# Performance work log

Hardware: AMD Instinct MI355X
Metric: run time of the kernel (lower is better)

## Reference

```python
import jax, jax.numpy as jnp
import numpy as np

N = 50000
E = 800000
C_IN, C_HID, C_OUT = 512, 128, 2
HEADS2 = 3
NEG_SLOPE = 0.2


def gat_conv(x, src, dst, W, att_src, att_dst, bias, heads, ch, concat):
    """PyG GATConv (eval mode) on pre-augmented (self-loop included) edge lists.
    x: [N, F_in], W: [F_in, heads*ch], att_*: [heads, ch], bias: [heads*ch] or [ch].
    """
    n = x.shape[0]
    h = (x @ W).reshape(n, heads, ch)                 # [N, H, C]
    a_src = (h * att_src).sum(-1)                     # [N, H]
    a_dst = (h * att_dst).sum(-1)                     # [N, H]
    e = jax.nn.leaky_relu(a_src[src] + a_dst[dst], NEG_SLOPE)  # [E', H]
    # segment softmax over edges sharing a destination node
    m = jax.ops.segment_max(e, dst, num_segments=n)
    m = jnp.where(jnp.isfinite(m), m, 0.0)
    ex = jnp.exp(e - m[dst])
    denom = jax.ops.segment_sum(ex, dst, num_segments=n)
    alpha = ex / (denom[dst] + 1e-16)                 # [E', H]
    out = jax.ops.segment_sum(h[src] * alpha[:, :, None], dst, num_segments=n)  # [N, H, C]
    out = out.reshape(n, heads * ch) if concat else out.mean(axis=1)
    return out + bias


def setup_inputs() -> dict:
    key = jax.random.key(0)
    ks = jax.random.split(key, 12)
    x = jax.random.normal(ks[0], (N, C_IN), dtype=jnp.float32)
    edge_index = jax.random.randint(ks[1], (2, E), 0, N, dtype=jnp.int64)
    s1 = 1.0 / np.sqrt(C_IN)
    s2 = 1.0 / np.sqrt(C_HID)
    return {
        "x": x,
        "edge_index": edge_index,
        "W1": jax.random.normal(ks[2], (C_IN, C_HID), dtype=jnp.float32) * s1,
        "att_src1": jax.random.normal(ks[3], (1, C_HID), dtype=jnp.float32) * s2,
        "att_dst1": jax.random.normal(ks[4], (1, C_HID), dtype=jnp.float32) * s2,
        "bias1": jnp.zeros((C_HID,), dtype=jnp.float32),
        "W2": jax.random.normal(ks[5], (C_HID, HEADS2 * C_OUT), dtype=jnp.float32) * s2,
        "att_src2": jax.random.normal(ks[6], (HEADS2, C_OUT), dtype=jnp.float32) * 0.5,
        "att_dst2": jax.random.normal(ks[7], (HEADS2, C_OUT), dtype=jnp.float32) * 0.5,
        "bias2": jnp.zeros((C_OUT,), dtype=jnp.float32),
    }


def reference(x, edge_index, W1, att_src1, att_dst1, bias1, W2, att_src2, att_dst2, bias2):
    n = x.shape[0]
    loop = jnp.arange(n, dtype=edge_index.dtype)
    src = jnp.concatenate([edge_index[0], loop])      # PyG add_self_loops=True
    dst = jnp.concatenate([edge_index[1], loop])
    h = gat_conv(x, src, dst, W1, att_src1, att_dst1, bias1, 1, C_HID, True)
    h = jax.nn.relu(h)                                # Dropout is identity in eval
    out = gat_conv(h, src, dst, W2, att_src2, att_dst2, bias2, HEADS2, C_OUT, False)
    return out
```

## Files before the change

### kernel.cpp

```cpp
#include <hip/hip_runtime.h>

#define N_NODES 50000
#define N_EDGES 800000
#define E_TOT   850000
#define C_IN    512
#define C_HID   128
#define NEG     0.2f

typedef _Float16 f16x8 __attribute__((ext_vector_type(8)));
typedef __attribute__((ext_vector_type(4))) float f32x4;

__device__ __forceinline__ float leaky(float x) { return x > 0.f ? x : NEG * x; }

union U32H2 { unsigned u; _Float16 h[2]; float f; };
union BFrag { uint4 u; f16x8 h; };

__device__ __forceinline__ unsigned short f2h(float f) {
  U32H2 c; c.h[0] = (_Float16)f; return (unsigned short)(c.u & 0xffff);
}

__device__ __forceinline__ unsigned pk2h(float a, float b) {
  union { __fp16 v __attribute__((ext_vector_type(2))); unsigned u; } c;
  c.v = __builtin_amdgcn_cvt_pkrtz(a, b);
  return c.u;
}

__global__ __launch_bounds__(256) void setup_kernel(
    const float* __restrict__ W1, const float* __restrict__ as1,
    const float* __restrict__ ad1, const int* __restrict__ ei,
    unsigned short* __restrict__ Wswz, float* __restrict__ v1s, float* __restrict__ v1d,
    int* __restrict__ deg, int* __restrict__ rnk) {
  const int b = blockIdx.x;
  if (b < 32) {
    int t = b * 256 + threadIdx.x;
    int c = t >> 6, kc = t & 63;
    if (c >= C_HID) return;
    int kblk = kc >> 2, q = kc & 3;
    int ct = c >> 4, l15 = c & 15;
    int lane = q * 16 + l15;
    unsigned short hb[8], lb[8];
#pragma unroll
    for (int i = 0; i < 8; i++) {
      float w = W1[(size_t)(kc * 8 + i) * C_HID + c];
      _Float16 hi = (_Float16)w;
      _Float16 lo = (_Float16)(w - (float)hi);
      U32H2 ch; ch.h[0] = hi;
      U32H2 cl; cl.h[0] = lo;
      hb[i] = (unsigned short)(ch.u & 0xffff);
      lb[i] = (unsigned short)(cl.u & 0xffff);
    }
    size_t chunk0 = ((size_t)(kblk * 8 + ct) * 2) * 512;
    *(uint4*)&Wswz[chunk0 + (size_t)lane * 8]       = *(uint4*)hb;
    *(uint4*)&Wswz[chunk0 + 512 + (size_t)lane * 8] = *(uint4*)lb;
  } else if (b < 160) {
    const int wv = threadIdx.x >> 6, lane = threadIdx.x & 63;
    const int k = (b - 32) * 4 + wv;
    if (k >= C_IN) return;
    float2 w = *(const float2*)(W1 + (size_t)k * C_HID + 2 * lane);
    float2 a = *(const float2*)(as1 + 2 * lane);
    float2 d = *(const float2*)(ad1 + 2 * lane);
    float s = w.x * a.x + w.y * a.y;
    float t = w.x * d.x + w.y * d.y;
#pragma unroll
    for (int m = 32; m >= 1; m >>= 1) {
      s += __shfl_xor(s, m, 64);
      t += __shfl_xor(t, m, 64);
    }
    if (lane == 0) { v1s[k] = s; v1d[k] = t; }
  } else {
    int e = (b - 160) * 256 + threadIdx.x;
    if (e < N_EDGES) rnk[e] = atomicAdd(&deg[ei[N_EDGES + e]], 1);
  }
}

__global__ __launch_bounds__(256) void lin1_kernel(const float* __restrict__ x,
    const unsigned short* __restrict__ Wswz,
    const float* __restrict__ v1s, const float* __restrict__ v1d,
    unsigned short* __restrict__ h1u, float* __restrict__ a_src, float* __restrict__ a_dst,
    const int* __restrict__ deg, int* __restrict__ rowptr) {
  __shared__ __attribute__((aligned(16))) unsigned short As[2][64][40];
  __shared__ int wsum[4];

  if (blockIdx.x == 0) {
    const int tid = threadIdx.x, lane = tid & 63, wv = tid >> 6;
    int carry = 0;
    for (int base = 0; base < N_NODES; base += 8192) {
      int i0 = base + tid * 32;
      int v[32];
      if (i0 + 32 <= N_NODES) {
#pragma unroll
        for (int k = 0; k < 8; k++) {
          int4 t4 = *(const int4*)(deg + i0 + 4 * k);
          v[4 * k]     = t4.x + 1; v[4 * k + 1] = t4.y + 1;
          v[4 * k + 2] = t4.z + 1; v[4 * k + 3] = t4.w + 1;
        }
      } else {
#pragma unroll
        for (int k = 0; k < 32; k++) v[k] = (i0 + k < N_NODES) ? deg[i0 + k] + 1 : 0;
      }
      int tsum = 0;
#pragma unroll
      for (int k = 0; k < 32; k++) tsum += v[k];
      int sc = tsum;
#pragma unroll
      for (int off = 1; off < 64; off <<= 1) {
        int t = __shfl_up(sc, off, 64);
        if (lane >= off) sc += t;
      }
      if (lane == 63) wsum[wv] = sc;
      __syncthreads();
      if (tid < 4) {
        int s = wsum[tid];
#pragma unroll
        for (int off = 1; off < 4; off <<= 1) {
          int t = __shfl_up(s, off, 64);
          if (tid >= off) s += t;
        }
        wsum[tid] = s;
      }
      __syncthreads();
      int run = carry + (wv ? wsum[wv - 1] : 0) + sc - tsum;
      if (i0 + 32 <= N_NODES) {
#pragma unroll
        for (int k = 0; k < 8; k++) {
          int4 w4;
          w4.x = run; run += v[4 * k];
          w4.y = run; run += v[4 * k + 1];
          w4.z = run; run += v[4 * k + 2];
          w4.w = run; run += v[4 * k + 3];
          *(int4*)(rowptr + i0 + 4 * k) = w4;
        }
      } else {
#pragma unroll
        for (int k = 0; k < 32; k++) {
          if (i0 + k < N_NODES) rowptr[i0 + k] = run;
          run += v[k];
        }
      }
      carry += wsum[3];
      __syncthreads();
    }
    if (tid == 0) rowptr[N_NODES] = carry;
    return;
  }

  const int tid  = threadIdx.x;
  const int lane = tid & 63, wv = tid >> 6;
  const int m0   = (blockIdx.x - 1) * 64;

  const int arow = tid >> 2, kseg = (tid & 3) * 8;
  int grow = m0 + arow;
  if (grow >= N_NODES) grow = N_NODES - 1;
  const float* xrow = x + (size_t)grow * C_IN + kseg;

  f32x4 acc[4][2];
#pragma unroll
  for (int rt = 0; rt < 4; rt++) { acc[rt][0] = (f32x4)0.f; acc[rt][1] = (f32x4)0.f; }
  float ps = 0.f, pd = 0.f;

  const int q = lane >> 4, l15 = lane & 15;

  float4 xa = *(const float4*)(xrow);
  float4 xb = *(const float4*)(xrow + 4);

#pragma unroll
  for (int kblk = 0; kblk < 16; kblk++) {
    const int k0 = kblk * 32;
    const int buf = kblk & 1;
    float4 vsa = *(const float4*)(v1s + k0 + kseg);
    float4 vsb = *(const float4*)(v1s + k0 + kseg + 4);
    float4 vda = *(const float4*)(v1d + k0 + kseg);
    float4 vdb = *(const float4*)(v1d + k0 + kseg + 4);
    ps += xa.x * vsa.x + xa.y * vsa.y + xa.z * vsa.z + xa.w * vsa.w
        + xb.x * vsb.x + xb.y * vsb.y + xb.z * vsb.z + xb.w * vsb.w;
    pd += xa.x * vda.x + xa.y * vda.y + xa.z * vda.z + xa.w * vda.w
        + xb.x * vdb.x + xb.y * vdb.y + xb.z * vdb.z + xb.w * vdb.w;
    *(uint4*)&As[buf][arow][kseg] = make_uint4(pk2h(xa.x, xa.y), pk2h(xa.z, xa.w),
                                               pk2h(xb.x, xb.y), pk2h(xb.z, xb.w));
    __syncthreads();
    if (kblk < 15) {
      xa = *(const float4*)(xrow + k0 + 32);
      xb = *(const float4*)(xrow + k0 + 36);
    }

    const unsigned short* bp = Wswz + ((size_t)(kblk * 8 + wv * 2) * 2) * 512 + (size_t)lane * 8;
    BFrag b00, b01, b10, b11;
    b00.u = *(const uint4*)(bp);
    b01.u = *(const uint4*)(bp + 512);
    b10.u = *(const uint4*)(bp + 1024);
    b11.u = *(const uint4*)(bp + 1536);

#pragma unroll
    for (int rt = 0; rt < 4; rt++) {
      f16x8 af = *(const f16x8*)&As[buf][rt * 16 + l15][q * 8];
      acc[rt][0] = __builtin_amdgcn_mfma_f32_16x16x32_f16(af, b00.h, acc[rt][0], 0, 0, 0);
      acc[rt][0] = __builtin_amdgcn_mfma_f32_16x16x32_f16(af, b01.h, acc[rt][0], 0, 0, 0);
      acc[rt][1] = __builtin_amdgcn_mfma_f32_16x16x32_f16(af, b10.h, acc[rt][1], 0, 0, 0);
      acc[rt][1] = __builtin_amdgcn_mfma_f32_16x16x32_f16(af, b11.h, acc[rt][1], 0, 0, 0);
    }
  }

  ps += __shfl_xor(ps, 1, 64); ps += __shfl_xor(ps, 2, 64);
  pd += __shfl_xor(pd, 1, 64); pd += __shfl_xor(pd, 2, 64);
  if ((tid & 3) == 0) {
    int row = m0 + arow;
    if (row < N_NODES) { a_src[row] = ps; a_dst[row] = pd; }
  }

#pragma unroll
  for (int rt = 0; rt < 4; rt++) {
    int rbase = m0 + rt * 16 + q * 4;
#pragma unroll
    for (int ct = 0; ct < 2; ct++) {
      int col = wv * 32 + ct * 16 + l15;
#pragma unroll
      for (int ri = 0; ri < 4; ri++) {
        int row = rbase + ri;
        if (row < N_NODES)
          h1u[(size_t)row * C_HID + col] = f2h(acc[rt][ct][ri]);
      }
    }
  }
}

__global__ void bucket_kernel(const int* __restrict__ ei, const int* __restrict__ rnk,
                              const int* __restrict__ rowptr,
                              const float* __restrict__ a_src, const float* __restrict__ a_dst,
                              int2* __restrict__ esw) {
  int e = blockIdx.x * blockDim.x + threadIdx.x;
  if (e >= E_TOT) return;
  int src, slot;
  if (e < N_EDGES) {
    src = ei[e];
    int dst = ei[N_EDGES + e];
    slot = rowptr[dst] + rnk[e];
    U32H2 c; c.f = __expf(leaky(a_src[src] + a_dst[dst]));
    esw[slot] = make_int2(src, (int)c.u);
  } else {
    int n = e - N_EDGES;
    slot = rowptr[n + 1] - 1;
    U32H2 c; c.f = __expf(leaky(a_src[n] + a_dst[n]));
    esw[slot] = make_int2(n, (int)c.u);
  }
}

__global__ __launch_bounds__(256) void agg1_kernel(const unsigned short* __restrict__ h1u,
    const int2* __restrict__ esw, const int* __restrict__ rowptr,
    const float* __restrict__ bias1, const float* __restrict__ W2,
    const float* __restrict__ as2w, const float* __restrict__ ad2w,
    float* __restrict__ hs2) {
  const int wv = threadIdx.x >> 6, lane = threadIdx.x & 63;
  const int q = lane >> 4, r = lane & 15;
  const int n = blockIdx.x * 4 + wv;
  const int start = rowptr[n], end = rowptr[n + 1];

  const unsigned short* hbase = h1u + r * 8;

  float acc[8] = {0, 0, 0, 0, 0, 0, 0, 0};
  float wsum = 0.f;
  for (int base = start; base < end; base += 64) {
    int idx = base + lane;
    int sreg = 0; float wreg = 0.f;
    if (idx < end) {
      int2 sv = esw[idx];
      sreg = sv.x;
      U32H2 c; c.u = (unsigned)sv.y;
      wreg = c.f;
    }
    wsum += wreg;
    const int cnt = min(64, end - base);

    auto batch = [&](int B) {
      int s[8]; float w[8];
#pragma unroll
      for (int j = 0; j < 8; j++) {
        int pos = B + j * 4 + q;
        s[j] = __shfl(sreg, pos, 64);
        w[j] = __shfl(wreg, pos, 64);
      }
      uint4 g[8];
#pragma unroll
      for (int j = 0; j < 8; j++)
        g[j] = *(const uint4*)(hbase + (size_t)s[j] * C_HID);
#pragma unroll
      for (int j = 0; j < 8; j++) {
        U32H2 c0, c1, c2, c3;
        c0.u = g[j].x; c1.u = g[j].y; c2.u = g[j].z; c3.u = g[j].w;
        const float W = w[j];
        acc[0] = fmaf(W, (float)c0.h[0], acc[0]); acc[1] = fmaf(W, (float)c0.h[1], acc[1]);
        acc[2] = fmaf(W, (float)c1.h[0], acc[2]); acc[3] = fmaf(W, (float)c1.h[1], acc[3]);
        acc[4] = fmaf(W, (float)c2.h[0], acc[4]); acc[5] = fmaf(W, (float)c2.h[1], acc[5]);
        acc[6] = fmaf(W, (float)c3.h[0], acc[6]); acc[7] = fmaf(W, (float)c3.h[1], acc[7]);
      }
    };
    batch(0);
    if (cnt > 32) batch(32);
  }

#pragma unroll
  for (int i = 0; i < 8; i++) {
    acc[i] += __shfl_xor(acc[i], 16, 64);
    acc[i] += __shfl_xor(acc[i], 32, 64);
  }
#pragma unroll
  for (int m = 32; m >= 1; m >>= 1) wsum += __shfl_xor(wsum, m, 64);
  const float inv = 1.f / wsum;

  float w2reg[8][6];
#pragma unroll
  for (int j = 0; j < 8; j++) {
    const float* w2r = W2 + (size_t)(r * 8 + j) * 6;
#pragma unroll
    for (int o = 0; o < 6; o++) w2reg[j][o] = w2r[o];
  }
  float4 ba = *(const float4*)(bias1 + r * 8);
  float4 bb = *(const float4*)(bias1 + r * 8 + 4);

  float u[8] = {fmaxf(acc[0] * inv + ba.x, 0.f), fmaxf(acc[1] * inv + ba.y, 0.f),
                fmaxf(acc[2] * inv + ba.z, 0.f), fmaxf(acc[3] * inv + ba.w, 0.f),
                fmaxf(acc[4] * inv + bb.x, 0.f), fmaxf(acc[5] * inv + bb.y, 0.f),
                fmaxf(acc[6] * inv + bb.z, 0.f), fmaxf(acc[7] * inv + bb.w, 0.f)};
  float p[6] = {0, 0, 0, 0, 0, 0};
#pragma unroll
  for (int j = 0; j < 8; j++)
#pragma unroll
    for (int o = 0; o < 6; o++) p[o] = fmaf(u[j], w2reg[j][o], p[o]);
#pragma unroll
  for (int o = 0; o < 6; o++) {
    p[o] += __shfl_xor(p[o], 1, 64);
    p[o] += __shfl_xor(p[o], 2, 64);
    p[o] += __shfl_xor(p[o], 4, 64);
    p[o] += __shfl_xor(p[o], 8, 64);
  }

  if (lane == 0) {
    float as0 = p[0] * as2w[0] + p[1] * as2w[1];
    float as1 = p[2] * as2w[2] + p[3] * as2w[3];
    float as2_ = p[4] * as2w[4] + p[5] * as2w[5];
    float ad0 = p[0] * ad2w[0] + p[1] * ad2w[1];
    float ad1 = p[2] * ad2w[2] + p[3] * ad2w[3];
    float ad2_ = p[4] * ad2w[4] + p[5] * ad2w[5];
    float* dst = hs2 + (size_t)n * 12;
    *(float4*)(dst)     = make_float4(p[0], p[1], p[2], p[3]);
    *(float4*)(dst + 4) = make_float4(p[4], p[5], as0, as1);
    *(float4*)(dst + 8) = make_float4(as2_, ad0, ad1, ad2_);
  }
}

__global__ __launch_bounds__(256) void agg2_kernel(const float* __restrict__ hs2,
    const int* __restrict__ rowptr, const int2* __restrict__ esw,
    const float* __restrict__ bias2, float* __restrict__ out) {
  const int wv = threadIdx.x >> 6, lane = threadIdx.x & 63;
  const int q = lane >> 4, r = lane & 15;
  const int n = blockIdx.x * 16 + wv * 4 + q;
  if (n >= N_NODES) return;
  const int start = rowptr[n], end = rowptr[n + 1];
  float4 own = *(const float4*)(hs2 + (size_t)n * 12 + 8);
  const float ad0 = own.y, ad1 = own.z, ad2 = own.w;

  float d0 = 0.f, d1 = 0.f, d2 = 0.f;
  float a0 = 0.f, a1 = 0.f, a2 = 0.f, a3 = 0.f, a4 = 0.f, a5 = 0.f;
  for (int j = start + r; j < end; j += 16) {
    int s = esw[j].x;
    const float* rec = hs2 + (size_t)s * 12;
    float4 A = *(const float4*)(rec);
    float4 B = *(const float4*)(rec + 4);
    float  C = rec[8];
    float e0 = __expf(leaky(B.z + ad0));
    float e1 = __expf(leaky(B.w + ad1));
    float e2 = __expf(leaky(C + ad2));
    d0 += e0; d1 += e1; d2 += e2;
    a0 += e0 * A.x; a1 += e0 * A.y;
    a2 += e1 * A.z; a3 += e1 * A.w;
    a4 += e2 * B.x; a5 += e2 * B.y;
  }
#pragma unroll
  for (int m = 8; m >= 1; m >>= 1) {
    d0 += __shfl_xor(d0, m, 64); d1 += __shfl_xor(d1, m, 64); d2 += __shfl_xor(d2, m, 64);
    a0 += __shfl_xor(a0, m, 64); a1 += __shfl_xor(a1, m, 64); a2 += __shfl_xor(a2, m, 64);
    a3 += __shfl_xor(a3, m, 64); a4 += __shfl_xor(a4, m, 64); a5 += __shfl_xor(a5, m, 64);
  }
  if (r == 0) {
    float o0 = (a0 / d0 + a2 / d1 + a4 / d2) * (1.f / 3.f) + bias2[0];
    float o1 = (a1 / d0 + a3 / d1 + a5 / d2) * (1.f / 3.f) + bias2[1];
    *(float2*)(out + (size_t)n * 2) = make_float2(o0, o1);
  }
}

extern "C" void kernel_launch(void* const* d_in, const int* in_sizes, int n_in,
                              void* d_out, int out_size, void* d_ws, size_t ws_size,
                              hipStream_t stream) {
  const float* x        = (const float*)d_in[0];
  const int*   ei       = (const int*)d_in[1];
  const float* W1       = (const float*)d_in[2];
  const float* att_src1 = (const float*)d_in[3];
  const float* att_dst1 = (const float*)d_in[4];
  const float* bias1    = (const float*)d_in[5];
  const float* W2       = (const float*)d_in[6];
  const float* att_src2 = (const float*)d_in[7];
  const float* att_dst2 = (const float*)d_in[8];
  const float* bias2    = (const float*)d_in[9];
  float* out = (float*)d_out;

  char* w = (char*)d_ws;
  auto alloc = [&](size_t bytes) {
    char* p = w;
    w += (bytes + 255) & ~(size_t)255;
    return p;
  };
  unsigned short* h1u    = (unsigned short*)alloc((size_t)N_NODES * C_HID * 2);
  unsigned short* Wswz   = (unsigned short*)alloc((size_t)C_IN * C_HID * 2 * 2);
  float*          v1s    = (float*)alloc((size_t)C_IN * 4);
  float*          v1d    = (float*)alloc((size_t)C_IN * 4);
  float*          a_src1 = (float*)alloc((size_t)N_NODES * 4);
  float*          a_dst1 = (float*)alloc((size_t)N_NODES * 4);
  int*            deg    = (int*)alloc((size_t)N_NODES * 4);
  int*            rowptr = (int*)alloc((size_t)(N_NODES + 4) * 4);
  int*            rnk    = (int*)alloc((size_t)N_EDGES * 4);
  int2*           esw    = (int2*)alloc((size_t)E_TOT * 8);
  float*          hs2    = (float*)alloc((size_t)N_NODES * 12 * 4);

  (void)hipMemsetAsync(deg, 0, (size_t)N_NODES * 4, stream);

  setup_kernel<<<160 + (N_EDGES + 255) / 256, 256, 0, stream>>>(
      W1, att_src1, att_dst1, ei, Wswz, v1s, v1d, deg, rnk);
  lin1_kernel<<<(N_NODES + 63) / 64 + 1, 256, 0, stream>>>(x, Wswz, v1s, v1d,
                                                           h1u, a_src1, a_dst1,
                                                           deg, rowptr);
  bucket_kernel<<<(E_TOT + 255) / 256, 256, 0, stream>>>(ei, rnk, rowptr,
                                                         a_src1, a_dst1, esw);
  agg1_kernel<<<N_NODES / 4, 256, 0, stream>>>(h1u, esw, rowptr, bias1, W2,
                                               att_src2, att_dst2, hs2);
  agg2_kernel<<<(N_NODES + 15) / 16, 256, 0, stream>>>(hs2, rowptr, esw, bias2, out);
}
```

Before: 320.8 us.

## Assign one node per 16-lane row in agg1 and use DPP row reductions

agg1 now maps each 16-lane row of a wavefront to its own destination node, so a wave handles four nodes at once. Each row loads its edge records directly, eight at a time, instead of staging them through lane shuffles, and the cross-row accumulator reduction is gone. The 16-lane sums in agg1 and agg2 are replaced with DPP row operations instead of ds_swizzle-based shuffles. The intent is to cut the shuffle and reduction overhead, which was high because the average degree (~17) left most of a 64-wide wave idle. In exchange, rows within a wave diverge on unequal degrees, and the 8-edge batch wastes loads on the tail.

```diff
diff --git a/kernel.cpp b/kernel.cpp
--- a/kernel.cpp
+++ b/kernel.cpp
@@ -23,6 +23,16 @@
   union { __fp16 v __attribute__((ext_vector_type(2))); unsigned u; } c;
   c.v = __builtin_amdgcn_cvt_pkrtz(a, b);
   return c.u;
+}
+
+__device__ __forceinline__ float row_reduce_add(float v) {
+  union { float f; int i; } a, b;
+  a.f = v;
+  b.i = __builtin_amdgcn_update_dpp(0, a.i, 0xB1, 0xF, 0xF, true);  a.f += b.f;
+  b.i = __builtin_amdgcn_update_dpp(0, a.i, 0x4E, 0xF, 0xF, true);  a.f += b.f;
+  b.i = __builtin_amdgcn_update_dpp(0, a.i, 0x124, 0xF, 0xF, true); a.f += b.f;
+  b.i = __builtin_amdgcn_update_dpp(0, a.i, 0x128, 0xF, 0xF, true); a.f += b.f;
+  return a.f;
 }
 
 __global__ __launch_bounds__(256) void setup_kernel(
@@ -250,90 +260,57 @@
     const float* __restrict__ as2w, const float* __restrict__ ad2w,
     float* __restrict__ hs2) {
   const int wv = threadIdx.x >> 6, lane = threadIdx.x & 63;
-  const int q = lane >> 4, r = lane & 15;
-  const int n = blockIdx.x * 4 + wv;
+  const int r = lane & 15;
+  const int n = blockIdx.x * 16 + wv * 4 + (lane >> 4);
   const int start = rowptr[n], end = rowptr[n + 1];
 
   const unsigned short* hbase = h1u + r * 8;
 
   float acc[8] = {0, 0, 0, 0, 0, 0, 0, 0};
   float wsum = 0.f;
-  for (int base = start; base < end; base += 64) {
-    int idx = base + lane;
-    int sreg = 0; float wreg = 0.f;
-    if (idx < end) {
-      int2 sv = esw[idx];
-      sreg = sv.x;
-      U32H2 c; c.u = (unsigned)sv.y;
-      wreg = c.f;
-    }
-    wsum += wreg;
-    const int cnt = min(64, end - base);
-
-    auto batch = [&](int B) {
-      int s[8]; float w[8];
-#pragma unroll
-      for (int j = 0; j < 8; j++) {
-        int pos = B + j * 4 + q;
-        s[j] = __shfl(sreg, pos, 64);
-        w[j] = __shfl(wreg, pos, 64);
-      }
-      uint4 g[8];
-#pragma unroll
-      for (int j = 0; j < 8; j++)
-        g[j] = *(const uint4*)(hbase + (size_t)s[j] * C_HID);
-#pragma unroll
-      for (int j = 0; j < 8; j++) {
-        U32H2 c0, c1, c2, c3;
-        c0.u = g[j].x; c1.u = g[j].y; c2.u = g[j].z; c3.u = g[j].w;
-        const float W = w[j];
-        acc[0] = fmaf(W, (float)c0.h[0], acc[0]); acc[1] = fmaf(W, (float)c0.h[1], acc[1]);
-        acc[2] = fmaf(W, (float)c1.h[0], acc[2]); acc[3] = fmaf(W, (float)c1.h[1], acc[3]);
-        acc[4] = fmaf(W, (float)c2.h[0], acc[4]); acc[5] = fmaf(W, (float)c2.h[1], acc[5]);
-        acc[6] = fmaf(W, (float)c3.h[0], acc[6]); acc[7] = fmaf(W, (float)c3.h[1], acc[7]);
-      }
-    };
-    batch(0);
-    if (cnt > 32) batch(32);
-  }
-
-#pragma unroll
-  for (int i = 0; i < 8; i++) {
-    acc[i] += __shfl_xor(acc[i], 16, 64);
-    acc[i] += __shfl_xor(acc[i], 32, 64);
-  }
-#pragma unroll
-  for (int m = 32; m >= 1; m >>= 1) wsum += __shfl_xor(wsum, m, 64);
+  for (int base = start; base < end; base += 8) {
+    const int cnt = end - base;
+    int2 rec[8];
+#pragma unroll
+    for (int j = 0; j < 8; j++)
+      rec[j] = esw[j < cnt ? base + j : base];
+    uint4 g[8];
+#pragma unroll
+    for (int j = 0; j < 8; j++)
+      g[j] = *(const uint4*)(hbase + (size_t)rec[j].x * C_HID);
+#pragma unroll
+    for (int j = 0; j < 8; j++) {
+      U32H2 cw; cw.u = (unsigned)rec[j].y;
+      const float W = (j < cnt) ? cw.f : 0.f;
+      wsum += W;
+      U32H2 c0, c1, c2, c3;
+      c0.u = g[j].x; c1.u = g[j].y; c2.u = g[j].z; c3.u = g[j].w;
+      acc[0] = fmaf(W, (float)c0.h[0], acc[0]); acc[1] = fmaf(W, (float)c0.h[1], acc[1]);
+      acc[2] = fmaf(W, (float)c1.h[0], acc[2]); acc[3] = fmaf(W, (float)c1.h[1], acc[3]);
+      acc[4] = fmaf(W, (float)c2.h[0], acc[4]); acc[5] = fmaf(W, (float)c2.h[1], acc[5]);
+      acc[6] = fmaf(W, (float)c3.h[0], acc[6]); acc[7] = fmaf(W, (float)c3.h[1], acc[7]);
+    }
+  }
+
   const float inv = 1.f / wsum;
 
-  float w2reg[8][6];
-#pragma unroll
-  for (int j = 0; j < 8; j++) {
-    const float* w2r = W2 + (size_t)(r * 8 + j) * 6;
-#pragma unroll
-    for (int o = 0; o < 6; o++) w2reg[j][o] = w2r[o];
-  }
   float4 ba = *(const float4*)(bias1 + r * 8);
   float4 bb = *(const float4*)(bias1 + r * 8 + 4);
-
   float u[8] = {fmaxf(acc[0] * inv + ba.x, 0.f), fmaxf(acc[1] * inv + ba.y, 0.f),
                 fmaxf(acc[2] * inv + ba.z, 0.f), fmaxf(acc[3] * inv + ba.w, 0.f),
                 fmaxf(acc[4] * inv + bb.x, 0.f), fmaxf(acc[5] * inv + bb.y, 0.f),
                 fmaxf(acc[6] * inv + bb.z, 0.f), fmaxf(acc[7] * inv + bb.w, 0.f)};
   float p[6] = {0, 0, 0, 0, 0, 0};
 #pragma unroll
-  for (int j = 0; j < 8; j++)
-#pragma unroll
-    for (int o = 0; o < 6; o++) p[o] = fmaf(u[j], w2reg[j][o], p[o]);
-#pragma unroll
-  for (int o = 0; o < 6; o++) {
-    p[o] += __shfl_xor(p[o], 1, 64);
-    p[o] += __shfl_xor(p[o], 2, 64);
-    p[o] += __shfl_xor(p[o], 4, 64);
-    p[o] += __shfl_xor(p[o], 8, 64);
-  }
-
-  if (lane == 0) {
+  for (int j = 0; j < 8; j++) {
+    const float* w2r = W2 + (size_t)(r * 8 + j) * 6;
+#pragma unroll
+    for (int o = 0; o < 6; o++) p[o] = fmaf(u[j], w2r[o], p[o]);
+  }
+#pragma unroll
+  for (int o = 0; o < 6; o++) p[o] = row_reduce_add(p[o]);
+
+  if (r == 0) {
     float as0 = p[0] * as2w[0] + p[1] * as2w[1];
     float as1 = p[2] * as2w[2] + p[3] * as2w[3];
     float as2_ = p[4] * as2w[4] + p[5] * as2w[5];
@@ -374,12 +351,9 @@
     a2 += e1 * A.z; a3 += e1 * A.w;
     a4 += e2 * B.x; a5 += e2 * B.y;
   }
-#pragma unroll
-  for (int m = 8; m >= 1; m >>= 1) {
-    d0 += __shfl_xor(d0, m, 64); d1 += __shfl_xor(d1, m, 64); d2 += __shfl_xor(d2, m, 64);
-    a0 += __shfl_xor(a0, m, 64); a1 += __shfl_xor(a1, m, 64); a2 += __shfl_xor(a2, m, 64);
-    a3 += __shfl_xor(a3, m, 64); a4 += __shfl_xor(a4, m, 64); a5 += __shfl_xor(a5, m, 64);
-  }
+  d0 = row_reduce_add(d0); d1 = row_reduce_add(d1); d2 = row_reduce_add(d2);
+  a0 = row_reduce_add(a0); a1 = row_reduce_add(a1); a2 = row_reduce_add(a2);
+  a3 = row_reduce_add(a3); a4 = row_reduce_add(a4); a5 = row_reduce_add(a5);
   if (r == 0) {
     float o0 = (a0 / d0 + a2 / d1 + a4 / d2) * (1.f / 3.f) + bias2[0];
     float o1 = (a1 / d0 + a3 / d1 + a5 / d2) * (1.f / 3.f) + bias2[1];
@@ -429,7 +403,7 @@
                                                            deg, rowptr);
   bucket_kernel<<<(E_TOT + 255) / 256, 256, 0, stream>>>(ei, rnk, rowptr,
                                                          a_src1, a_dst1, esw);
-  agg1_kernel<<<N_NODES / 4, 256, 0, stream>>>(h1u, esw, rowptr, bias1, W2,
-                                               att_src2, att_dst2, hs2);
+  agg1_kernel<<<N_NODES / 16, 256, 0, stream>>>(h1u, esw, rowptr, bias1, W2,
+                                                att_src2, att_dst2, hs2);
   agg2_kernel<<<(N_NODES + 15) / 16, 256, 0, stream>>>(hs2, rowptr, esw, bias2, out);
 }
```

After: 293.2 us. 8.6% less time.
